# Performance work log

Hardware: AMD Instinct MI355X
Metric: run time of the kernel (lower is better)

Reference implementation:

```python
import jax, jax.numpy as jnp
import numpy as np

N = 8192       # number of nodes
T = 4          # number of edge types
E = 131072     # edges per type
D = 32         # edge_emb_dim
H = 4          # num_head_attentions
NEG_SLOPE = 0.2


def setup_inputs() -> dict:
    key = jax.random.key(0)
    k1, k2, k3, k4 = jax.random.split(key, 4)
    scores = jax.random.normal(k1, (N, 1), dtype=jnp.float32)
    edge_type_emb = jax.random.normal(k2, (T, D), dtype=jnp.float32)
    edge_index = jax.random.randint(k3, (T, 2, E), 0, N, dtype=jnp.int32)
    # xavier-normal-ish init for the per-head attention weights [H, D+2, 1]
    std = float(np.sqrt(2.0 / (D + 2 + 1)))
    attention_weight = jax.random.normal(k4, (H, D + 2, 1), dtype=jnp.float32) * std
    return {"scores": scores, "edge_type_emb": edge_type_emb,
            "edge_index": edge_index, "attention_weight": attention_weight}


def _head_forward(W_h, scores, edge_type_emb, src, tgt):
    # W_h: [D+2, 1]; split the concat-matmul: cat([s_src, emb, s_tgt]) @ W
    w = W_h[:, 0]
    w_src, w_emb, w_tgt = w[0], w[1:D + 1], w[D + 1]
    s = scores[:, 0]                               # [N]
    # per-edge attention logits, vectorized over edge types: [T, E]
    emb_term = edge_type_emb @ w_emb               # [T]
    vals = s[src] * w_src + s[tgt] * w_tgt + emb_term[:, None]
    # scatter-add into dense NxN (duplicates accumulate, matching += semantics)
    A = jnp.zeros((N, N), dtype=scores.dtype).at[src.ravel(), tgt.ravel()].add(vals.ravel())
    A = jnp.where(A >= 0, A, NEG_SLOPE * A)        # LeakyReLU(0.2)
    A = jax.nn.softmax(A, axis=-1)                 # dense row softmax
    return A @ scores                               # [N, 1]


def reference(scores, edge_type_emb, edge_index, attention_weight):
    src = edge_index[:, 0, :]  # [T, E]
    tgt = edge_index[:, 1, :]
    head_fn = lambda W_h: _head_forward(W_h, scores, edge_type_emb, src, tgt)
    outs = jax.vmap(head_fn)(attention_weight)      # [H, N, 1]
    return jnp.mean(outs, axis=0)                   # [N, 1]
```

## Files before the change

kernel.cpp:

```cpp
#include <hip/hip_runtime.h>
#include <stdint.h>


#define NN 8192
#define TT 4
#define EE 131072
#define DD 32
#define HH 4
#define NEG_SLOPE 0.2f

#define NB    2048
#define RPB   4
#define SEG   128
#define ABLK  256
#define CAPBB 12
#define A_EPT 8
#define EMPTY 0xFFFFFFFFu


__global__ void __launch_bounds__(256) kA(const int* __restrict__ ei,
                                          const float* __restrict__ scores,
                                          const float* __restrict__ ete,
                                          const float* __restrict__ aw,
                                          uint8_t* __restrict__ cnt,
                                          uint32_t* __restrict__ buf,
                                          float* __restrict__ f) {
    int tid = threadIdx.x;
    if (blockIdx.x == ABLK) {
        __shared__ float red[256];
        float s = 0.f;
        for (int i = tid; i < NN; i += 256) s += scores[i];
        red[tid] = s;
        __syncthreads();
        for (int off = 128; off > 0; off >>= 1) {
            if (tid < off) red[tid] += red[tid + off];
            __syncthreads();
        }
        if (tid == 0) f[0] = red[0];
        if (tid < HH) {
            f[1 + tid] = aw[tid * (DD + 2)];
            f[5 + tid] = aw[tid * (DD + 2) + DD + 1];
        }
        if (tid < HH * TT) {
            int h = tid / TT, t = tid % TT;
            float acc = 0.f;
            for (int d = 0; d < DD; ++d)
                acc += ete[t * DD + d] * aw[h * (DD + 2) + 1 + d];
            f[9 + tid] = acc;
        }
        return;
    }

    __shared__ uint32_t hist[NB];
    for (int i = tid; i < NB; i += 256) hist[i] = 0;
    __syncthreads();

    uint32_t gtid = blockIdx.x * 256u + (uint32_t)tid;
    uint32_t t  = gtid >> 14;
    uint32_t e0 = (gtid & 16383u) * A_EPT;
    const int4* sp = (const int4*)(ei + (size_t)(t * 2) * EE + e0);
    const int4* tp = (const int4*)(ei + (size_t)(t * 2 + 1) * EE + e0);

    uint32_t val[A_EPT];
    uint32_t rnk[A_EPT];
    #pragma unroll
    for (int k = 0; k < A_EPT / 4; ++k) {
        int4 s4 = sp[k];
        int4 t4 = tp[k];
        val[k*4+0] = ((uint32_t)s4.x << 15) | ((uint32_t)t4.x << 2) | t;
        val[k*4+1] = ((uint32_t)s4.y << 15) | ((uint32_t)t4.y << 2) | t;
        val[k*4+2] = ((uint32_t)s4.z << 15) | ((uint32_t)t4.z << 2) | t;
        val[k*4+3] = ((uint32_t)s4.w << 15) | ((uint32_t)t4.w << 2) | t;
    }
    #pragma unroll
    for (int k = 0; k < A_EPT; ++k)
        rnk[k] = atomicAdd(&hist[val[k] >> 17], 1u);
    __syncthreads();

    for (int i = tid; i < NB; i += 256) {
        uint32_t c = hist[i];
        cnt[(uint32_t)i * ABLK + blockIdx.x] = (uint8_t)(c > CAPBB ? CAPBB : c);
    }
    #pragma unroll
    for (int k = 0; k < A_EPT; ++k) {
        if (rnk[k] < CAPBB) {
            uint32_t b = val[k] >> 17;
            buf[((size_t)b * ABLK + blockIdx.x) * CAPBB + rnk[k]] = val[k] & 0x1FFFFu;
        }
    }
}

__global__ void __launch_bounds__(256) kB(const float* __restrict__ scores,
                                          const uint8_t* __restrict__ cnt,
                                          const uint32_t* __restrict__ buf,
                                          const float* __restrict__ f,
                                          float* __restrict__ out) {
    __shared__ uint32_t tab[RPB * SEG];
    __shared__ uint8_t  cc[ABLK];
    int tid = threadIdx.x;
    for (int i = tid; i < RPB * SEG; i += 256) tab[i] = EMPTY;
    uint32_t b = blockIdx.x;
    cc[tid] = cnt[b * ABLK + tid];

    float st = f[0];
    float wsrc[HH], wtgt[HH], em[HH * TT];
    #pragma unroll
    for (int h = 0; h < HH; ++h) { wsrc[h] = f[1 + h]; wtgt[h] = f[5 + h]; }
    #pragma unroll
    for (int k = 0; k < HH * TT; ++k) em[k] = f[9 + k];
    __syncthreads();

    const uint32_t* rb = buf + ((size_t)b * ABLK + tid) * CAPBB;
    int c = cc[tid];
    for (int i = 0; i < c; ++i) {
        uint32_t v   = rb[i];
        uint32_t row = (v >> 15) & 3u;
        uint32_t tgt = (v >> 2) & 8191u;
        uint32_t tt  = v & 3u;
        uint32_t inc = 1u << (13 + 4 * tt);
        uint32_t fresh = tgt | inc;
        uint32_t pos = (tgt * 2654435761u) >> 25;
        uint32_t base = row * SEG;
        while (true) {
            uint32_t cur = atomicCAS(&tab[base + pos], EMPTY, fresh);
            if (cur == EMPTY) break;
            bool done = false;
            while ((cur & 0x1FFFu) == tgt) {
                uint32_t prev = atomicCAS(&tab[base + pos], cur, cur + inc);
                if (prev == cur) { done = true; break; }
                cur = prev;
            }
            if (done) break;
            pos = (pos + 1) & (SEG - 1);
        }
    }
    __syncthreads();

    int wave = tid >> 6, lane = tid & 63;
    int r = wave;
    float si = scores[b * RPB + r];
    float num[HH] = {0.f, 0.f, 0.f, 0.f};
    float den[HH] = {0.f, 0.f, 0.f, 0.f};
    #pragma unroll
    for (int half = 0; half < 2; ++half) {
        uint32_t w = tab[r * SEG + half * 64 + lane];
        if (w != EMPTY) {
            uint32_t tgt = w & 0x1FFFu;
            float c0 = (float)((w >> 13) & 15u);
            float c1 = (float)((w >> 17) & 15u);
            float c2 = (float)((w >> 21) & 15u);
            float c3 = (float)((w >> 25) & 15u);
            float ctot = c0 + c1 + c2 + c3;
            float sj = scores[tgt];
            #pragma unroll
            for (int h = 0; h < HH; ++h) {
                float a = ctot * (si * wsrc[h] + sj * wtgt[h])
                        + c0 * em[h * 4 + 0] + c1 * em[h * 4 + 1]
                        + c2 * em[h * 4 + 2] + c3 * em[h * 4 + 3];
                a = (a >= 0.f) ? a : NEG_SLOPE * a;
                float ex = __expf(a) - 1.f;
                den[h] += ex;
                num[h] += ex * sj;
            }
        }
    }
    #pragma unroll
    for (int m = 32; m > 0; m >>= 1) {
        #pragma unroll
        for (int h = 0; h < HH; ++h) {
            num[h] += __shfl_xor(num[h], m, 64);
            den[h] += __shfl_xor(den[h], m, 64);
        }
    }
    if (lane == 0) {
        float acc = 0.f;
        #pragma unroll
        for (int h = 0; h < HH; ++h)
            acc += (st + num[h]) / ((float)NN + den[h]);
        out[b * RPB + r] = acc * (1.f / HH);
    }
}

extern "C" void kernel_launch(void* const* d_in, const int* in_sizes, int n_in,
                              void* d_out, int out_size, void* d_ws, size_t ws_size,
                              hipStream_t stream) {
    const float* scores = (const float*)d_in[0];
    const float* ete    = (const float*)d_in[1];
    const int*   ei     = (const int*)d_in[2];
    const float* aw     = (const float*)d_in[3];
    float* out = (float*)d_out;

    uint8_t*  cnt = (uint8_t*)d_ws;
    float*    f   = (float*)((char*)d_ws + (size_t)NB * ABLK);
    uint32_t* buf = (uint32_t*)((char*)d_ws + (size_t)NB * ABLK + 1024);

    kA<<<ABLK + 1, 256, 0, stream>>>(ei, scores, ete, aw, cnt, buf, f);
    kB<<<NB, 256, 0, stream>>>(scores, cnt, buf, f, out);
}
```

Before: 97.86 us.

## Replace fixed-capacity bucket slots with compacted per-block CSR regions

```diff
diff --git a/kernel.cpp b/kernel.cpp
--- a/kernel.cpp
+++ b/kernel.cpp
@@ -9,12 +9,13 @@
 #define HH 4
 #define NEG_SLOPE 0.2f
 
-#define NB    2048
-#define RPB   4
-#define SEG   128
-#define ABLK  256
-#define CAPBB 12
+#define NB   2048
+#define RPB  4
+#define SEG  128
+#define ABLK 256
+#define EPB  2048
 #define A_EPT 8
+#define REGB 12288
 #define EMPTY 0xFFFFFFFFu
 
 
@@ -22,8 +23,7 @@
                                           const float* __restrict__ scores,
                                           const float* __restrict__ ete,
                                           const float* __restrict__ aw,
-                                          uint8_t* __restrict__ cnt,
-                                          uint32_t* __restrict__ buf,
+                                          char* __restrict__ regs,
                                           float* __restrict__ f) {
     int tid = threadIdx.x;
     if (blockIdx.x == ABLK) {
@@ -52,7 +52,12 @@
     }
 
     __shared__ uint32_t hist[NB];
-    for (int i = tid; i < NB; i += 256) hist[i] = 0;
+    __shared__ uint32_t offs[NB];
+    __shared__ uint32_t stage[EPB];
+    __shared__ uint32_t wsum[256];
+
+    #pragma unroll
+    for (int j = 0; j < NB / 256; ++j) hist[tid + j * 256] = 0;
     __syncthreads();
 
     uint32_t gtid = blockIdx.x * 256u + (uint32_t)tid;
@@ -77,30 +82,52 @@
         rnk[k] = atomicAdd(&hist[val[k] >> 17], 1u);
     __syncthreads();
 
-    for (int i = tid; i < NB; i += 256) {
-        uint32_t c = hist[i];
-        cnt[(uint32_t)i * ABLK + blockIdx.x] = (uint8_t)(c > CAPBB ? CAPBB : c);
-    }
-    #pragma unroll
-    for (int k = 0; k < A_EPT; ++k) {
-        if (rnk[k] < CAPBB) {
-            uint32_t b = val[k] >> 17;
-            buf[((size_t)b * ABLK + blockIdx.x) * CAPBB + rnk[k]] = val[k] & 0x1FFFFu;
-        }
-    }
+    uint32_t loc[NB / 256];
+    uint32_t lsum = 0;
+    #pragma unroll
+    for (int j = 0; j < NB / 256; ++j) {
+        loc[j] = lsum;
+        lsum += hist[tid * (NB / 256) + j];
+    }
+    wsum[tid] = lsum;
+    __syncthreads();
+    for (int off = 1; off < 256; off <<= 1) {
+        uint32_t u = (tid >= off) ? wsum[tid - off] : 0u;
+        __syncthreads();
+        wsum[tid] += u;
+        __syncthreads();
+    }
+    uint32_t base = (tid == 0) ? 0u : wsum[tid - 1];
+    #pragma unroll
+    for (int j = 0; j < NB / 256; ++j)
+        offs[tid * (NB / 256) + j] = base + loc[j];
+    __syncthreads();
+
+    #pragma unroll
+    for (int k = 0; k < A_EPT; ++k)
+        stage[offs[val[k] >> 17] + rnk[k]] = val[k] & 0x1FFFFu;
+    __syncthreads();
+
+    char* reg = regs + (size_t)blockIdx.x * REGB;
+    uint16_t* h16 = (uint16_t*)reg;
+    uint32_t* dat = (uint32_t*)(reg + 4096);
+    #pragma unroll
+    for (int j = 0; j < NB / 256; ++j)
+        h16[tid * (NB / 256) + j] = (uint16_t)offs[tid * (NB / 256) + j];
+    #pragma unroll
+    for (int j = 0; j < EPB / 256; ++j)
+        dat[j * 256 + tid] = stage[j * 256 + tid];
 }
 
 __global__ void __launch_bounds__(256) kB(const float* __restrict__ scores,
-                                          const uint8_t* __restrict__ cnt,
-                                          const uint32_t* __restrict__ buf,
+                                          const char* __restrict__ regs,
                                           const float* __restrict__ f,
                                           float* __restrict__ out) {
     __shared__ uint32_t tab[RPB * SEG];
-    __shared__ uint8_t  cc[ABLK];
     int tid = threadIdx.x;
-    for (int i = tid; i < RPB * SEG; i += 256) tab[i] = EMPTY;
+    tab[tid] = EMPTY;
+    tab[tid + 256] = EMPTY;
     uint32_t b = blockIdx.x;
-    cc[tid] = cnt[b * ABLK + tid];
 
     float st = f[0];
     float wsrc[HH], wtgt[HH], em[HH * TT];
@@ -110,23 +137,26 @@
     for (int k = 0; k < HH * TT; ++k) em[k] = f[9 + k];
     __syncthreads();
 
-    const uint32_t* rb = buf + ((size_t)b * ABLK + tid) * CAPBB;
-    int c = cc[tid];
-    for (int i = 0; i < c; ++i) {
-        uint32_t v   = rb[i];
+    const char* reg = regs + (size_t)tid * REGB;
+    const uint16_t* h16 = (const uint16_t*)reg;
+    const uint32_t* dat = (const uint32_t*)(reg + 4096);
+    uint32_t off = h16[b];
+    uint32_t nxt = (b == NB - 1) ? (uint32_t)EPB : (uint32_t)h16[b + 1];
+    for (uint32_t i = off; i < nxt; ++i) {
+        uint32_t v   = dat[i];
         uint32_t row = (v >> 15) & 3u;
         uint32_t tgt = (v >> 2) & 8191u;
         uint32_t tt  = v & 3u;
         uint32_t inc = 1u << (13 + 4 * tt);
         uint32_t fresh = tgt | inc;
         uint32_t pos = (tgt * 2654435761u) >> 25;
-        uint32_t base = row * SEG;
+        uint32_t hb = row * SEG;
         while (true) {
-            uint32_t cur = atomicCAS(&tab[base + pos], EMPTY, fresh);
+            uint32_t cur = atomicCAS(&tab[hb + pos], EMPTY, fresh);
             if (cur == EMPTY) break;
             bool done = false;
             while ((cur & 0x1FFFu) == tgt) {
-                uint32_t prev = atomicCAS(&tab[base + pos], cur, cur + inc);
+                uint32_t prev = atomicCAS(&tab[hb + pos], cur, cur + inc);
                 if (prev == cur) { done = true; break; }
                 cur = prev;
             }
@@ -190,10 +220,9 @@
     const float* aw     = (const float*)d_in[3];
     float* out = (float*)d_out;
 
-    uint8_t*  cnt = (uint8_t*)d_ws;
-    float*    f   = (float*)((char*)d_ws + (size_t)NB * ABLK);
-    uint32_t* buf = (uint32_t*)((char*)d_ws + (size_t)NB * ABLK + 1024);
-
-    kA<<<ABLK + 1, 256, 0, stream>>>(ei, scores, ete, aw, cnt, buf, f);
-    kB<<<NB, 256, 0, stream>>>(scores, cnt, buf, f, out);
+    float* f    = (float*)d_ws;
+    char*  regsp = (char*)d_ws + 256;
+
+    kA<<<ABLK + 1, 256, 0, stream>>>(ei, scores, ete, aw, regsp, f);
+    kB<<<NB, 256, 0, stream>>>(scores, regsp, f, out);
 }
```

After: 95.82 us. -2.1%, faster.
